# Kernel optimization log

Hardware: AMD Instinct MI355X
Metric: run time of the kernel (lower is better)

## Reference

```python
import jax, jax.numpy as jnp
import numpy as np

N_NODES = 100000
N_EDGES = 3200000
G_EDGES = 1600000
D_FEAT = 256
K_CLUSTERS = 16
COLLAPSE_REG = 0.1


def setup_inputs() -> dict:
    key = jax.random.key(0)
    ks = jax.random.split(key, 12)
    inp = {
        'features': jax.random.normal(ks[0], (N_NODES, D_FEAT), dtype=jnp.float32),
        'W': jax.random.normal(ks[1], (D_FEAT, K_CLUSTERS), dtype=jnp.float32) / np.sqrt(D_FEAT),
        'b': jnp.zeros((K_CLUSTERS,), dtype=jnp.float32),
        'adj_src': jax.random.randint(ks[2], (N_EDGES,), 0, N_NODES, dtype=jnp.int32),
        'adj_dst': jax.random.randint(ks[3], (N_EDGES,), 0, N_NODES, dtype=jnp.int32),
        'adj_val': jax.random.uniform(ks[4], (N_EDGES,), dtype=jnp.float32),
        'g1_src': jax.random.randint(ks[5], (G_EDGES,), 0, N_NODES, dtype=jnp.int32),
        'g1_dst': jax.random.randint(ks[6], (G_EDGES,), 0, N_NODES, dtype=jnp.int32),
        'g1_val': jax.random.uniform(ks[7], (G_EDGES,), dtype=jnp.float32),
        'g2_src': jax.random.randint(ks[8], (G_EDGES,), 0, N_NODES, dtype=jnp.int32),
        'g2_dst': jax.random.randint(ks[9], (G_EDGES,), 0, N_NODES, dtype=jnp.int32),
        'g2_val': jax.random.uniform(ks[10], (G_EDGES,), dtype=jnp.float32),
        'lamda': 1,
    }
    return inp


def _spmm(src, dst, val, X, n):
    # (sparse A) @ X where A[src, dst] = val : out[i] = sum_j A[i,j] X[j]
    return jax.ops.segment_sum(val[:, None] * X[dst], src, num_segments=n)


def _col_degrees(src, dst, val, n):
    # tf.sparse.reduce_sum(A, axis=0): column sums
    return jax.ops.segment_sum(val, dst, num_segments=n)


def reference(features, W, b, adj_src, adj_dst, adj_val,
              g1_src, g1_dst, g1_val, g2_src, g2_dst, g2_val, lamda):
    n = features.shape[0]
    k = W.shape[1]
    # soft cluster assignments  [n, k]
    S = jax.nn.softmax(features @ W + b, axis=1)
    cluster_sizes = jnp.sum(S, axis=0)            # [k]
    S_pool = S / cluster_sizes                    # [n, k]

    # full-graph modularity
    deg = _col_degrees(adj_src, adj_dst, adj_val, n)  # [n]
    m = jnp.sum(deg)                                  # total edge weight
    AS = _spmm(adj_src, adj_dst, adj_val, S, n)       # [n, k]
    graph_pooled = AS.T @ S                           # [k, k]
    dS = deg @ S                                      # [k] = S^T deg
    normalizer = jnp.outer(dS, dS) / 2.0 / m          # [k, k]
    spectral_loss = -jnp.trace(graph_pooled - normalizer) / 2.0 / m

    # per-group modularity Q_g
    def group_Q(src, dst, val):
        gdeg = _col_degrees(src, dst, val, n)
        gm = jnp.sum(gdeg)
        safe_gm = jnp.where(gm > 0, gm, 1.0)
        gAS = _spmm(src, dst, val, S, n)
        g_pooled = gAS.T @ S
        gdS = gdeg @ S
        g_norm = jnp.outer(gdS, gdS) / 2.0 / safe_gm
        Qg = jnp.trace(g_pooled - g_norm) / 2.0 / m
        return jnp.where(gm > 0, Qg, 0.0), gm

    Q1, m1 = group_Q(g1_src, g1_dst, g1_val)
    Q2, m2 = group_Q(g2_src, g2_dst, g2_val)
    Q_min = jnp.minimum(Q1, Q2)
    g_edges_mean = (m1 + m2) / 2.0
    edge_ratio = m / (g_edges_mean + 1e-8)
    fairness_loss = edge_ratio * (-Q_min)

    collapse_loss = (jnp.linalg.norm(cluster_sizes) / n) * jnp.sqrt(jnp.float32(k)) - 1.0

    total_loss = spectral_loss + lamda * fairness_loss + COLLAPSE_REG * collapse_loss

    features_pooled = jax.nn.selu(S_pool.T @ features)  # [k, d]
    return features_pooled, S, total_loss
```

## Files before the change

### kernel.cpp

```cpp
#include <hip/hip_runtime.h>
#include <cstddef>
#include <cstdint>


#define G1_MAX   1024
#define EGRID    2048
#define NSEG     16
#define OFF_E    0
#define SZ_E     (3 * 18 * EGRID)
#define OFF_R    (OFF_E + SZ_E)
#define OFF_G    (OFF_R + 4112)
#define OFF_F8   (OFF_G + 64)

#define TROWS    32
#define RSTR     264

#define BLK0     1024
#define BLK12    512

typedef int      iv4  __attribute__((ext_vector_type(4)));
typedef float    fv4  __attribute__((ext_vector_type(4)));
typedef unsigned uv4  __attribute__((ext_vector_type(4)));
typedef _Float16 hh;
typedef hh       h2   __attribute__((ext_vector_type(2)));
typedef hh       h8   __attribute__((ext_vector_type(8)));
typedef float    f32x4 __attribute__((ext_vector_type(4)));

#if __has_builtin(__builtin_amdgcn_cvt_pk_f32_fp8)
#define HW_FP8 1
#endif

__device__ __forceinline__ h2 bch2(unsigned u) { return __builtin_bit_cast(h2, u); }

__device__ __forceinline__ unsigned pk16u(float x, float y)
{
#if __has_builtin(__builtin_amdgcn_cvt_pkrtz)
    return __builtin_bit_cast(unsigned, __builtin_amdgcn_cvt_pkrtz(x, y));
#else
    h2 r; r[0] = (hh)x; r[1] = (hh)y; return __builtin_bit_cast(unsigned, r);
#endif
}
__device__ __forceinline__ unsigned short h16(float x)
{
    return (unsigned short)(pk16u(x, 0.f) & 0xFFFFu);
}

__device__ __forceinline__ unsigned f32_to_e4m3(float f)
{
    unsigned bits = __float_as_uint(f);
    unsigned s = bits >> 31;
    int e32 = (int)((bits >> 23) & 255);
    unsigned m23 = bits & 0x7FFFFF;
    int e = e32 - 120;
    unsigned out;
    if (e32 == 0) out = 0;
    else if (e <= 0) {
        float av = fabsf(f);
        int q = (int)(av * 512.0f + 0.5f);
        out = (unsigned)q;
    } else if (e > 15) out = (15u << 3) | 6u;
    else {
        unsigned m3 = (m23 + 0x80000u) >> 20;
        if (m3 == 8u) { m3 = 0u; ++e; if (e > 15) { e = 15; m3 = 6u; } }
        out = ((unsigned)e << 3) | m3;
    }
    return out | (s << 7);
}

__device__ __forceinline__ void decode16(uint4 r, float* o, const float* lut)
{
#ifdef HW_FP8
    #pragma unroll
    for (int j = 0; j < 4; ++j) {
        unsigned u = (&r.x)[j];
        auto lo = __builtin_amdgcn_cvt_pk_f32_fp8(u, false);
        auto hi = __builtin_amdgcn_cvt_pk_f32_fp8(u, true);
        o[4*j]   = lo[0]; o[4*j+1] = lo[1];
        o[4*j+2] = hi[0]; o[4*j+3] = hi[1];
    }
#else
    #pragma unroll
    for (int j = 0; j < 4; ++j) {
        unsigned u = (&r.x)[j];
        #pragma unroll
        for (int q = 0; q < 4; ++q)
            o[4*j+q] = lut[(u >> (8*q)) & 255];
    }
#endif
}

__global__ void __launch_bounds__(256)
k_rows(const float* __restrict__ F, const float* __restrict__ W,
       const float* __restrict__ b, float* __restrict__ S_out,
       unsigned* __restrict__ S_f8, float* __restrict__ ws_P, int n, int n_tiles)
{
    __shared__ unsigned short Wt_u16[16][RSTR];
    __shared__ unsigned short rows_u16[TROWS][RSTR];
    __shared__ float S_lds[TROWS][17];
    __shared__ float Sred[2][16][17];
    __shared__ float cs_red[256];

    const int t = threadIdx.x;
    const int w = t >> 6;
    const int l = t & 63;
    const int l15 = l & 15;
    const int lg  = l >> 4;

    for (int idx = t; idx < 4096; idx += 256) {
        int k = idx >> 4, nn = idx & 15;
        Wt_u16[nn][k] = h16(W[idx]);
    }
    const float bk = b[l15];

    f32x4 pacc[4];
    #pragma unroll
    for (int j = 0; j < 4; ++j) pacc[j] = (f32x4){0.f, 0.f, 0.f, 0.f};
    float cs_acc = 0.f;

    float4 stg[8];
    auto load_tile = [&](int tl) {
        const float4* F4 = (const float4*)(F + (size_t)tl * TROWS * 256);
        #pragma unroll
        for (int q = 0; q < 8; ++q) {
            int r = (t >> 6) + 4 * q;
            float4 z = {0.f, 0.f, 0.f, 0.f};
            stg[q] = (tl * TROWS + r < n) ? F4[t + (q << 8)] : z;
        }
    };
    if (blockIdx.x < (unsigned)n_tiles) load_tile(blockIdx.x);
    __syncthreads();

    for (int tile = blockIdx.x; tile < n_tiles; tile += gridDim.x) {
        const int c4 = t & 63;
        #pragma unroll
        for (int q = 0; q < 8; ++q) {
            int r = (t >> 6) + 4 * q;
            unsigned u0 = pk16u(stg[q].x, stg[q].y);
            unsigned u1 = pk16u(stg[q].z, stg[q].w);
            *(uint2*)&rows_u16[r][c4 << 2] = make_uint2(u0, u1);
        }
        __syncthreads();

        {
            int nt2 = tile + gridDim.x;
            if (nt2 < n_tiles) load_tile(nt2);
        }

        const int mt  = w & 1;
        const int ks0 = (w >> 1) * 4;
        f32x4 c0 = (f32x4){0.f, 0.f, 0.f, 0.f};
        #pragma unroll
        for (int s = 0; s < 4; ++s) {
            int k0 = (ks0 + s) << 5;
            uv4 av = *(const uv4*)&rows_u16[(mt << 4) + l15][k0 + (lg << 3)];
            uv4 bv = *(const uv4*)&Wt_u16[l15][k0 + (lg << 3)];
            c0 = __builtin_amdgcn_mfma_f32_16x16x32_f16(
                     __builtin_bit_cast(h8, av), __builtin_bit_cast(h8, bv),
                     c0, 0, 0, 0);
        }
        if (w >= 2) {
            #pragma unroll
            for (int p = 0; p < 4; ++p)
                Sred[mt][(lg << 2) + p][l15] = c0[p];
        }
        __syncthreads();

        if (w < 2) {
            float lv[4];
            #pragma unroll
            for (int p = 0; p < 4; ++p)
                lv[p] = c0[p] + Sred[mt][(lg << 2) + p][l15] + bk;
            float mx[4], sm[4];
            #pragma unroll
            for (int p = 0; p < 4; ++p) mx[p] = lv[p];
            #pragma unroll
            for (int o = 8; o; o >>= 1)
                #pragma unroll
                for (int p = 0; p < 4; ++p)
                    mx[p] = fmaxf(mx[p], __shfl_xor(mx[p], o));
            #pragma unroll
            for (int p = 0; p < 4; ++p) { lv[p] = __expf(lv[p] - mx[p]); sm[p] = lv[p]; }
            #pragma unroll
            for (int o = 8; o; o >>= 1)
                #pragma unroll
                for (int p = 0; p < 4; ++p)
                    sm[p] += __shfl_xor(sm[p], o);
            int rbase = tile * TROWS + (mt << 4) + (lg << 2);
            #pragma unroll
            for (int p = 0; p < 4; ++p) {
                float sv = lv[p] / sm[p];
                S_lds[(mt << 4) + (lg << 2) + p][l15] = sv;
                if (rbase + p < n) cs_acc += sv;
            }
        }
        __syncthreads();

        if (t < 128) {
            int r = t >> 2, c = t & 3;
            int row = tile * TROWS + r;
            if (row < n) {
                float v0 = S_lds[r][4*c + 0];
                float v1 = S_lds[r][4*c + 1];
                float v2 = S_lds[r][4*c + 2];
                float v3 = S_lds[r][4*c + 3];
                *(float4*)&S_out[((size_t)row << 4) + 4*c] = make_float4(v0, v1, v2, v3);
                unsigned u = f32_to_e4m3(v0) | (f32_to_e4m3(v1) << 8)
                           | (f32_to_e4m3(v2) << 16) | (f32_to_e4m3(v3) << 24);
                S_f8[((size_t)row << 2) + c] = u;
            }
        }

        {
            float a0 = S_lds[(lg << 3) + 0][l15];
            float a1 = S_lds[(lg << 3) + 1][l15];
            float a2 = S_lds[(lg << 3) + 2][l15];
            float a3 = S_lds[(lg << 3) + 3][l15];
            float a4 = S_lds[(lg << 3) + 4][l15];
            float a5 = S_lds[(lg << 3) + 5][l15];
            float a6 = S_lds[(lg << 3) + 6][l15];
            float a7 = S_lds[(lg << 3) + 7][l15];
            uv4 au;
            au[0] = pk16u(a0, a1); au[1] = pk16u(a2, a3);
            au[2] = pk16u(a4, a5); au[3] = pk16u(a6, a7);
            h8 ah = __builtin_bit_cast(h8, au);

            #pragma unroll
            for (int j = 0; j < 4; ++j) {
                int nc = (w << 2) + j;
                int dcol = (nc << 4) + l15;
                unsigned short b0 = rows_u16[(lg << 3) + 0][dcol];
                unsigned short b1 = rows_u16[(lg << 3) + 1][dcol];
                unsigned short b2 = rows_u16[(lg << 3) + 2][dcol];
                unsigned short b3 = rows_u16[(lg << 3) + 3][dcol];
                unsigned short b4 = rows_u16[(lg << 3) + 4][dcol];
                unsigned short b5 = rows_u16[(lg << 3) + 5][dcol];
                unsigned short b6 = rows_u16[(lg << 3) + 6][dcol];
                unsigned short b7 = rows_u16[(lg << 3) + 7][dcol];
                uv4 bu;
                bu[0] = (unsigned)b0 | ((unsigned)b1 << 16);
                bu[1] = (unsigned)b2 | ((unsigned)b3 << 16);
                bu[2] = (unsigned)b4 | ((unsigned)b5 << 16);
                bu[3] = (unsigned)b6 | ((unsigned)b7 << 16);
                pacc[j] = __builtin_amdgcn_mfma_f32_16x16x32_f16(
                              ah, __builtin_bit_cast(h8, bu), pacc[j], 0, 0, 0);
            }
        }
        __syncthreads();
    }

    {
        float* dst = ws_P + (size_t)blockIdx.x * 4112;
        #pragma unroll
        for (int j = 0; j < 4; ++j)
            #pragma unroll
            for (int p = 0; p < 4; ++p)
                dst[((lg << 2) + p) * 256 + (w << 6) + (j << 4) + l15] = pacc[j][p];
    }
    cs_red[t] = cs_acc;
    __syncthreads();
    if (t < 16) {
        float ssum = 0.f;
        #pragma unroll
        for (int i = 0; i < 16; ++i) ssum += cs_red[t + (i << 4)];
        ws_P[(size_t)blockIdx.x * 4112 + 4096 + t] = ssum;
    }
}

__global__ void __launch_bounds__(256)
k_reduce(const float* __restrict__ ws_P, float* __restrict__ ws_red, int nb)
{
    const int seg  = blockIdx.x & (NSEG - 1);
    const int jblk = blockIdx.x / NSEG;
    const int idx  = jblk * 256 + threadIdx.x;
    if (idx >= 4112) return;
    const int chunk = (nb + NSEG - 1) / NSEG;
    const int b0 = seg * chunk;
    const int b1 = min(nb, b0 + chunk);
    float s = 0.f;
    for (int bb = b0; bb < b1; ++bb)
        s += ws_P[(size_t)bb * 4112 + idx];
    atomicAdd(&ws_red[idx], s);
}

__global__ void __launch_bounds__(256, 4)
k_edge(const int* __restrict__ src0, const int* __restrict__ dst0,
       const float* __restrict__ val0, int n0,
       const int* __restrict__ src1, const int* __restrict__ dst1,
       const float* __restrict__ val1, int n1,
       const int* __restrict__ src2, const int* __restrict__ dst2,
       const float* __restrict__ val2, int n2,
       const uint4* __restrict__ S8, float* __restrict__ ws_e,
       int b0, int b1)
{
#ifndef HW_FP8
    __shared__ float lut[256];
    if (threadIdx.x < 256) {
        int i = threadIdx.x;
        int e_ = (i >> 3) & 15, m_ = i & 7, s_ = i >> 7;
        float v = e_ ? ldexpf((float)(8 + m_), e_ - 10) : ldexpf((float)m_, -9);
        lut[i] = s_ ? -v : v;
    }
    __syncthreads();
    const float* lutp = lut;
#else
    const float* lutp = nullptr;
#endif

    int g, bb, nblk, nE;
    const int* src; const int* dst; const float* val;
    if ((int)blockIdx.x < b0)      { g = 0; bb = blockIdx.x;      nblk = b0;             src = src0; dst = dst0; val = val0; nE = n0; }
    else if ((int)blockIdx.x < b1) { g = 1; bb = blockIdx.x - b0; nblk = b1 - b0;        src = src1; dst = dst1; val = val1; nE = n1; }
    else                           { g = 2; bb = blockIdx.x - b1; nblk = gridDim.x - b1; src = src2; dst = dst2; val = val2; nE = n2; }

    float m_acc = 0.f, tr_acc = 0.f;
    float gds[16];
    #pragma unroll
    for (int k = 0; k < 16; ++k) gds[k] = 0.f;

    const int nv = nE >> 2;
    const iv4* s4 = (const iv4*)src;
    const iv4* d4 = (const iv4*)dst;
    const fv4* v4 = (const fv4*)val;
    const int stride = nblk * 256;

    for (int i = bb * 256 + threadIdx.x; i < nv; i += stride) {
        iv4 sa = __builtin_nontemporal_load(&s4[i]);
        iv4 da = __builtin_nontemporal_load(&d4[i]);
        fv4 va = __builtin_nontemporal_load(&v4[i]);
        uint4 rs[4], rd[4];
        #pragma unroll
        for (int e = 0; e < 4; ++e) {
            rs[e] = S8[sa[e]];
            rd[e] = S8[da[e]];
        }
        #pragma unroll
        for (int e = 0; e < 4; ++e) {
            float sv[16], dv[16];
            decode16(rs[e], sv, lutp);
            decode16(rd[e], dv, lutp);
            float v = va[e];
            float dot = 0.f;
            #pragma unroll
            for (int k = 0; k < 16; ++k) dot = fmaf(sv[k], dv[k], dot);
            m_acc += v;
            tr_acc = fmaf(v, dot, tr_acc);
            #pragma unroll
            for (int k = 0; k < 16; ++k) gds[k] = fmaf(v, dv[k], gds[k]);
        }
    }

    if (bb == 0) {
        int e = (nv << 2) + threadIdx.x;
        if (e < nE) {
            float sv[16], dv[16];
            decode16(S8[src[e]], sv, lutp);
            decode16(S8[dst[e]], dv, lutp);
            float v = val[e];
            float dot = 0.f;
            #pragma unroll
            for (int k = 0; k < 16; ++k) dot = fmaf(sv[k], dv[k], dot);
            m_acc += v;
            tr_acc = fmaf(v, dot, tr_acc);
            #pragma unroll
            for (int k = 0; k < 16; ++k) gds[k] = fmaf(v, dv[k], gds[k]);
        }
    }

    #pragma unroll
    for (int o = 32; o; o >>= 1) {
        m_acc  += __shfl_xor(m_acc, o);
        tr_acc += __shfl_xor(tr_acc, o);
        #pragma unroll
        for (int k = 0; k < 16; ++k) gds[k] += __shfl_xor(gds[k], o);
    }
    __shared__ float wred[4][18];
    const int wid = threadIdx.x >> 6, lane = threadIdx.x & 63;
    if (lane == 0) {
        wred[wid][0] = m_acc; wred[wid][1] = tr_acc;
        #pragma unroll
        for (int k = 0; k < 16; ++k) wred[wid][2 + k] = gds[k];
    }
    __syncthreads();
    if (threadIdx.x < 18) {
        float s = wred[0][threadIdx.x] + wred[1][threadIdx.x]
                + wred[2][threadIdx.x] + wred[3][threadIdx.x];
        ws_e[(size_t)g * 18 * EGRID + (size_t)threadIdx.x * EGRID + bb] = s;
    }
}

__global__ void __launch_bounds__(256)
k_ereduce(const float* __restrict__ ws_e, float* __restrict__ G54,
          int g0, int g1, int g2)
{
    const int p = blockIdx.x;
    const int g = p / 18, slot = p % 18;
    int grids[3] = {g0, g1, g2};
    const int gb = grids[g];
    const float* base = ws_e + (size_t)g * 18 * EGRID + (size_t)slot * EGRID;

    const int t = threadIdx.x;
    float s = 0.f;
    for (int bb = t; bb < gb; bb += 256) s += base[bb];
    #pragma unroll
    for (int o = 32; o; o >>= 1) s += __shfl_xor(s, o);

    __shared__ float wr[4];
    if ((t & 63) == 0) wr[t >> 6] = s;
    __syncthreads();
    if (t == 0) G54[p] = wr[0] + wr[1] + wr[2] + wr[3];
}

__global__ void __launch_bounds__(256)
k_final(const float* __restrict__ ws_red, const float* __restrict__ G54,
        const void* __restrict__ lamda_ptr, float* __restrict__ out, int n)
{
    __shared__ float G[54];
    const int t = threadIdx.x;
    if (t < 54) G[t] = G54[t];
    __syncthreads();

    const float* P  = ws_red;
    const float* cs = ws_red + 4096;

    const float scale = 1.0507009873554805f;
    const float alpha = 1.6732632423543772f;
    for (int idx = t; idx < 4096; idx += 256) {
        int k = idx >> 8;
        float x = P[idx] / cs[k];
        float y = x > 0.f ? scale * x : scale * alpha * (expf(x) - 1.f);
        out[idx] = y;
    }

    if (t == 0) {
        int   li = *(const int*)lamda_ptr;
        float lf = *(const float*)lamda_ptr;
        float lamda = (li > -100000 && li < 100000) ? (float)li : lf;

        float m = G[0], trA = G[1];
        float ds2 = 0.f;
        for (int k = 0; k < 16; ++k) ds2 += G[2 + k] * G[2 + k];
        float spectral = -(trA - ds2 / (2.f * m)) / (2.f * m);

        float Q[2], gm[2];
        for (int g = 0; g < 2; ++g) {
            const float* Gg = G + 18 * (g + 1);
            float mg = Gg[0], trg = Gg[1];
            float gds2 = 0.f;
            for (int k = 0; k < 16; ++k) gds2 += Gg[2 + k] * Gg[2 + k];
            float safe = mg > 0.f ? mg : 1.f;
            float q = (trg - gds2 / (2.f * safe)) / (2.f * m);
            Q[g]  = mg > 0.f ? q : 0.f;
            gm[g] = mg;
        }
        float Qmin = fminf(Q[0], Q[1]);
        float gmean = 0.5f * (gm[0] + gm[1]);
        float fairness = (m / (gmean + 1e-8f)) * (-Qmin);

        float csn = 0.f;
        for (int k = 0; k < 16; ++k) csn += cs[k] * cs[k];
        float collapse = (sqrtf(csn) / (float)n) * 4.f - 1.f;

        out[4096 + (size_t)n * 16] = spectral + lamda * fairness + 0.1f * collapse;
    }
}

extern "C" void kernel_launch(void* const* d_in, const int* in_sizes, int n_in,
                              void* d_out, int out_size, void* d_ws, size_t ws_size,
                              hipStream_t stream)
{
    const float* F       = (const float*)d_in[0];
    const float* W       = (const float*)d_in[1];
    const float* b       = (const float*)d_in[2];
    const int*   adj_src = (const int*)d_in[3];
    const int*   adj_dst = (const int*)d_in[4];
    const float* adj_val = (const float*)d_in[5];
    const int*   g1_src  = (const int*)d_in[6];
    const int*   g1_dst  = (const int*)d_in[7];
    const float* g1_val  = (const float*)d_in[8];
    const int*   g2_src  = (const int*)d_in[9];
    const int*   g2_dst  = (const int*)d_in[10];
    const float* g2_val  = (const float*)d_in[11];
    const void*  lamda_p = d_in[12];

    const int n  = in_sizes[0] / 256;
    const int nE = in_sizes[3];
    const int n1 = in_sizes[6];
    const int n2 = in_sizes[9];

    float* out   = (float*)d_out;
    float* S_out = out + 4096;

    float* ws   = (float*)d_ws;
    float* ws_e = ws + OFF_E;
    float* ws_r = ws + OFF_R;
    float* ws_g = ws + OFF_G;
    unsigned* S8 = (unsigned*)(ws + OFF_F8);
    const size_t off_p = (size_t)OFF_F8 + (size_t)n * 4;
    float* ws_P = ws + off_p;

    const int n_tiles = (n + TROWS - 1) / TROWS;
    long avail = ((long)(ws_size / 4) - (long)off_p) / 4112;
    int grid1 = n_tiles < G1_MAX ? n_tiles : G1_MAX;
    if (avail < grid1) grid1 = (int)avail;
    if (grid1 < 1) grid1 = 1;

    (void)hipMemsetAsync(ws_r, 0, 4112 * sizeof(float), stream);

    k_rows<<<grid1, 256, 0, stream>>>(F, W, b, S_out, S8, ws_P, n, n_tiles);
    k_reduce<<<17 * NSEG, 256, 0, stream>>>(ws_P, ws_r, grid1);

    const int b0 = BLK0, b1g = BLK12, b2g = BLK12;
    k_edge<<<b0 + b1g + b2g, 256, 0, stream>>>(
        adj_src, adj_dst, adj_val, nE,
        g1_src, g1_dst, g1_val, n1,
        g2_src, g2_dst, g2_val, n2,
        (const uint4*)S8, ws_e, b0, b0 + b1g);

    k_ereduce<<<54, 256, 0, stream>>>(ws_e, ws_g, b0, b1g, b2g);
    k_final<<<1, 256, 0, stream>>>(ws_r, ws_g, lamda_p, out, n);
}
```

Measured before the change: 140.1 us.

## Double row tile to 64 and give each wave a full-K logits MFMA

The per-block row tile in k_rows grows from 32 to 64 rows. Each of the four waves now computes the full 256-long K reduction for its own 16-row slice, instead of splitting K across wave pairs. This removes the Sred LDS partial-sum exchange and one __syncthreads per tile, lets all waves run the softmax, and amortizes barriers and W setup over more rows. The costs are a doubled register staging buffer (16 float4 per thread) and more LDS use, which could lower occupancy.

```diff
diff --git a/kernel.cpp b/kernel.cpp
--- a/kernel.cpp
+++ b/kernel.cpp
@@ -12,7 +12,7 @@
 #define OFF_G    (OFF_R + 4112)
 #define OFF_F8   (OFF_G + 64)
 
-#define TROWS    32
+#define TROWS    64
 #define RSTR     264
 
 #define BLK0     1024
@@ -29,8 +29,6 @@
 #if __has_builtin(__builtin_amdgcn_cvt_pk_f32_fp8)
 #define HW_FP8 1
 #endif
-
-__device__ __forceinline__ h2 bch2(unsigned u) { return __builtin_bit_cast(h2, u); }
 
 __device__ __forceinline__ unsigned pk16u(float x, float y)
 {
@@ -97,7 +95,6 @@
     __shared__ unsigned short Wt_u16[16][RSTR];
     __shared__ unsigned short rows_u16[TROWS][RSTR];
     __shared__ float S_lds[TROWS][17];
-    __shared__ float Sred[2][16][17];
     __shared__ float cs_red[256];
 
     const int t = threadIdx.x;
@@ -117,12 +114,12 @@
     for (int j = 0; j < 4; ++j) pacc[j] = (f32x4){0.f, 0.f, 0.f, 0.f};
     float cs_acc = 0.f;
 
-    float4 stg[8];
+    float4 stg[16];
     auto load_tile = [&](int tl) {
         const float4* F4 = (const float4*)(F + (size_t)tl * TROWS * 256);
         #pragma unroll
-        for (int q = 0; q < 8; ++q) {
-            int r = (t >> 6) + 4 * q;
+        for (int q = 0; q < 16; ++q) {
+            int r = w + 4 * q;
             float4 z = {0.f, 0.f, 0.f, 0.f};
             stg[q] = (tl * TROWS + r < n) ? F4[t + (q << 8)] : z;
         }
@@ -131,10 +128,10 @@
     __syncthreads();
 
     for (int tile = blockIdx.x; tile < n_tiles; tile += gridDim.x) {
-        const int c4 = t & 63;
-        #pragma unroll
-        for (int q = 0; q < 8; ++q) {
-            int r = (t >> 6) + 4 * q;
+        const int c4 = l;
+        #pragma unroll
+        for (int q = 0; q < 16; ++q) {
+            int r = w + 4 * q;
             unsigned u0 = pk16u(stg[q].x, stg[q].y);
             unsigned u1 = pk16u(stg[q].z, stg[q].w);
             *(uint2*)&rows_u16[r][c4 << 2] = make_uint2(u0, u1);
@@ -146,33 +143,21 @@
             if (nt2 < n_tiles) load_tile(nt2);
         }
 
-        const int mt  = w & 1;
-        const int ks0 = (w >> 1) * 4;
         f32x4 c0 = (f32x4){0.f, 0.f, 0.f, 0.f};
         #pragma unroll
-        for (int s = 0; s < 4; ++s) {
-            int k0 = (ks0 + s) << 5;
-            uv4 av = *(const uv4*)&rows_u16[(mt << 4) + l15][k0 + (lg << 3)];
+        for (int s = 0; s < 8; ++s) {
+            int k0 = s << 5;
+            uv4 av = *(const uv4*)&rows_u16[(w << 4) + l15][k0 + (lg << 3)];
             uv4 bv = *(const uv4*)&Wt_u16[l15][k0 + (lg << 3)];
             c0 = __builtin_amdgcn_mfma_f32_16x16x32_f16(
                      __builtin_bit_cast(h8, av), __builtin_bit_cast(h8, bv),
                      c0, 0, 0, 0);
         }
-        if (w >= 2) {
-            #pragma unroll
-            for (int p = 0; p < 4; ++p)
-                Sred[mt][(lg << 2) + p][l15] = c0[p];
-        }
-        __syncthreads();
-
-        if (w < 2) {
-            float lv[4];
-            #pragma unroll
-            for (int p = 0; p < 4; ++p)
-                lv[p] = c0[p] + Sred[mt][(lg << 2) + p][l15] + bk;
-            float mx[4], sm[4];
-            #pragma unroll
-            for (int p = 0; p < 4; ++p) mx[p] = lv[p];
+
+        {
+            float lv[4], mx[4], sm[4];
+            #pragma unroll
+            for (int p = 0; p < 4; ++p) { lv[p] = c0[p] + bk; mx[p] = lv[p]; }
             #pragma unroll
             for (int o = 8; o; o >>= 1)
                 #pragma unroll
@@ -185,17 +170,17 @@
                 #pragma unroll
                 for (int p = 0; p < 4; ++p)
                     sm[p] += __shfl_xor(sm[p], o);
-            int rbase = tile * TROWS + (mt << 4) + (lg << 2);
+            int rbase = tile * TROWS + (w << 4) + (lg << 2);
             #pragma unroll
             for (int p = 0; p < 4; ++p) {
                 float sv = lv[p] / sm[p];
-                S_lds[(mt << 4) + (lg << 2) + p][l15] = sv;
+                S_lds[(w << 4) + (lg << 2) + p][l15] = sv;
                 if (rbase + p < n) cs_acc += sv;
             }
         }
         __syncthreads();
 
-        if (t < 128) {
+        {
             int r = t >> 2, c = t & 3;
             int row = tile * TROWS + r;
             if (row < n) {
@@ -210,15 +195,17 @@
             }
         }
 
-        {
-            float a0 = S_lds[(lg << 3) + 0][l15];
-            float a1 = S_lds[(lg << 3) + 1][l15];
-            float a2 = S_lds[(lg << 3) + 2][l15];
-            float a3 = S_lds[(lg << 3) + 3][l15];
-            float a4 = S_lds[(lg << 3) + 4][l15];
-            float a5 = S_lds[(lg << 3) + 5][l15];
-            float a6 = S_lds[(lg << 3) + 6][l15];
-            float a7 = S_lds[(lg << 3) + 7][l15];
+        #pragma unroll
+        for (int ks = 0; ks < 2; ++ks) {
+            int rb = (ks << 5) + (lg << 3);
+            float a0 = S_lds[rb + 0][l15];
+            float a1 = S_lds[rb + 1][l15];
+            float a2 = S_lds[rb + 2][l15];
+            float a3 = S_lds[rb + 3][l15];
+            float a4 = S_lds[rb + 4][l15];
+            float a5 = S_lds[rb + 5][l15];
+            float a6 = S_lds[rb + 6][l15];
+            float a7 = S_lds[rb + 7][l15];
             uv4 au;
             au[0] = pk16u(a0, a1); au[1] = pk16u(a2, a3);
             au[2] = pk16u(a4, a5); au[3] = pk16u(a6, a7);
@@ -226,16 +213,15 @@
 
             #pragma unroll
             for (int j = 0; j < 4; ++j) {
-                int nc = (w << 2) + j;
-                int dcol = (nc << 4) + l15;
-                unsigned short b0 = rows_u16[(lg << 3) + 0][dcol];
-                unsigned short b1 = rows_u16[(lg << 3) + 1][dcol];
-                unsigned short b2 = rows_u16[(lg << 3) + 2][dcol];
-                unsigned short b3 = rows_u16[(lg << 3) + 3][dcol];
-                unsigned short b4 = rows_u16[(lg << 3) + 4][dcol];
-                unsigned short b5 = rows_u16[(lg << 3) + 5][dcol];
-                unsigned short b6 = rows_u16[(lg << 3) + 6][dcol];
-                unsigned short b7 = rows_u16[(lg << 3) + 7][dcol];
+                int dcol = (((w << 2) + j) << 4) + l15;
+                unsigned short b0 = rows_u16[rb + 0][dcol];
+                unsigned short b1 = rows_u16[rb + 1][dcol];
+                unsigned short b2 = rows_u16[rb + 2][dcol];
+                unsigned short b3 = rows_u16[rb + 3][dcol];
+                unsigned short b4 = rows_u16[rb + 4][dcol];
+                unsigned short b5 = rows_u16[rb + 5][dcol];
+                unsigned short b6 = rows_u16[rb + 6][dcol];
+                unsigned short b7 = rows_u16[rb + 7][dcol];
                 uv4 bu;
                 bu[0] = (unsigned)b0 | ((unsigned)b1 << 16);
                 bu[1] = (unsigned)b2 | ((unsigned)b3 << 16);
```

Result: no change. 141.5 us (+1.0%).
